# Kernel optimization log

Measured on AMD Instinct MI355X. Metric: run time of the kernel, lower is better.

Reference implementation:

```python
import jax, jax.numpy as jnp
import numpy as np

B, N, C_IN, C_OUT, BASIS = 8, 128, 64, 64, 15
AVG_NOBJ = 49.0
NEG_SLOPE = 0.01  # torch LeakyReLU default


def eops_2_to_2_sum(x, average_nobj=AVG_NOBJ):
    """x: [B, C, N, N] -> [B, C, 15, N, N].
    5 order-zero ops + 10 sum-aggregation ops (sums normalized by average_nobj,
    double sums by average_nobj**2, as in PELICAN's 'sum' aggregation)."""
    n = x.shape[-1]
    eye = jnp.eye(n, dtype=x.dtype)                       # [N, N]
    d = jnp.diagonal(x, axis1=-2, axis2=-1)               # [B, C, N]
    rowsum = x.sum(-1) / average_nobj                      # [B, C, N]
    colsum = x.sum(-2) / average_nobj                      # [B, C, N]
    trace = d.sum(-1) / average_nobj                       # [B, C]
    allsum = x.sum((-2, -1)) / (average_nobj ** 2)         # [B, C]
    bc = lambda v: jnp.broadcast_to(v, x.shape)
    ops = [
        # --- order zero (no aggregation) ---
        d[..., :, None] * eye,                 # diag(A) embedded on diagonal
        bc(d[..., :, None]),                   # A_ii broadcast along j
        bc(d[..., None, :]),                   # A_jj broadcast along i
        x,                                     # identity
        jnp.swapaxes(x, -1, -2),               # transpose
        # --- aggregation ops ---
        rowsum[..., :, None] * eye,            # row sums on diagonal
        colsum[..., :, None] * eye,            # col sums on diagonal
        trace[..., None, None] * eye,          # trace on diagonal
        allsum[..., None, None] * eye,         # total sum on diagonal
        bc(rowsum[..., :, None]),              # rowsum_i broadcast along j
        bc(rowsum[..., None, :]),              # rowsum_j broadcast along i
        bc(colsum[..., :, None]),              # colsum_i broadcast along j
        bc(colsum[..., None, :]),              # colsum_j broadcast along i
        bc(trace[..., None, None]),            # trace broadcast everywhere
        bc(allsum[..., None, None]),           # total sum broadcast everywhere
    ]
    return jnp.stack(ops, axis=2)              # [B, C, 15, N, N]


def setup_inputs() -> dict:
    key = jax.random.key(0)
    ks = jax.random.split(key, 5)
    inputs = jax.random.normal(ks[0], (B, N, N, C_IN), jnp.float32)
    mask = jnp.ones((B, N, N, 1), jnp.float32)
    nobj = jnp.full((B,), float(N), jnp.float32)
    s_b = float(np.sqrt(1.0 / BASIS))
    s_d = float(np.sqrt(1.0 / C_IN))
    coefs00 = jax.random.normal(ks[1], (C_IN, BASIS), jnp.float32) * s_b
    coefs01 = jax.random.normal(ks[2], (C_OUT, BASIS), jnp.float32) * s_b
    coefs10 = jax.random.normal(ks[3], (C_IN, C_OUT), jnp.float32) * s_d
    coefs11 = jax.random.normal(ks[4], (C_IN, C_OUT), jnp.float32) * s_d
    bias = jnp.zeros((C_OUT,), jnp.float32)
    diag_bias = jnp.zeros((C_OUT,), jnp.float32)
    return {"inputs": inputs, "mask": mask, "nobj": nobj,
            "coefs00": coefs00, "coefs01": coefs01,
            "coefs10": coefs10, "coefs11": coefs11,
            "bias": bias, "diag_bias": diag_bias}


def reference(inputs, mask, nobj, coefs00, coefs01, coefs10, coefs11, bias, diag_bias):
    # inputs: [B, N, N, C_in] -> channels-first for basis construction
    x = jnp.transpose(inputs, (0, 3, 1, 2))                     # [B, C, N, N]
    ops = eops_2_to_2_sum(x)                                    # [B, C, 15, N, N]
    # low-rank reconstructed coefficient tensor [C_in, C_out, 15]
    coefs = (coefs00[:, None, :] * coefs10[:, :, None]
             + coefs01[None, :, :] * coefs11[:, :, None])
    out = jnp.einsum('dsb,ndbij->nijs', coefs, ops)             # [B, N, N, C_out]
    eye = jnp.eye(inputs.shape[1], dtype=out.dtype)[None, :, :, None]
    out = out + bias[None, None, None, :] + eye * diag_bias[None, None, None, :]
    out = jax.nn.leaky_relu(out, NEG_SLOPE)
    return out * mask
```

## Files before the change

kernel.cpp:

```cpp
#include <hip/hip_runtime.h>

#define BB 8
#define NN 128
#define CC 64
static constexpr float INV_A = 1.0f / 49.0f;

#define OFF_C    0
#define OFF_CB   61440
#define OFF_RS   65536
#define OFF_CS   131072
#define OFF_DV   196608
#define OFF_U1   263168
#define OFF_U2   328704
#define OFF_DG   394240
#define OFF_XT   459776

typedef __attribute__((ext_vector_type(8))) short v8s;
typedef __attribute__((ext_vector_type(4))) float v4f;

static __device__ inline unsigned pack2bf(float a, float b) {
    union { float f; unsigned u; } ua, ub; ua.f = a; ub.f = b;
    return ((ua.u + 0x8000u) >> 16) | ((ub.u + 0x8000u) & 0xffff0000u);
}
static __device__ inline unsigned short f2bf(float a) {
    union { float f; unsigned u; } ua; ua.f = a;
    return (unsigned short)((ua.u + 0x8000u) >> 16);
}

__global__ void k_pre(const float* __restrict__ in,
                      const float* __restrict__ c00, const float* __restrict__ c01,
                      const float* __restrict__ c10, const float* __restrict__ c11,
                      float* __restrict__ ws) {
    if (blockIdx.x >= 512) {
        int idx = (blockIdx.x - 512) * 256 + threadIdx.x;
        if (idx < 15 * 4096) {
            int b = idx >> 12; int r = idx & 4095; int d = r >> 6; int s = r & 63;
            ws[OFF_C + idx] = c00[d * 15 + b] * c10[d * 64 + s] + c01[s * 15 + b] * c11[d * 64 + s];
        } else if (idx < 15 * 4096 + 8192) {
            int k = idx - 15 * 4096;
            int which = k >> 12;
            int r = k & 4095; int s = r >> 6; int d = r & 63;
            int b = 3 + which;
            float v = c00[d * 15 + b] * c10[d * 64 + s] + c01[s * 15 + b] * c11[d * 64 + s];
            unsigned short* cb = (unsigned short*)(ws + OFF_CB);
            cb[s * 128 + which * 64 + d] = f2bf(v);
        }
        return;
    }
    __shared__ float4 part[4][4][16];
    int mode = blockIdx.x >> 8;
    int bb = blockIdx.x & 255;
    int n = bb >> 5; int g0 = (bb & 31) * 4;
    int t = threadIdx.x;
    int q = t >> 6; int ii = (t >> 4) & 3; int d4 = t & 15;
    float4 acc = make_float4(0.f, 0.f, 0.f, 0.f);
    if (mode == 0) {
        int i = g0 + ii;
        float4 dvv = acc; bool hd = false;
        const float* base = in + ((size_t)(n * NN + i)) * NN * CC + d4 * 4;
        for (int j = q * 32; j < q * 32 + 32; ++j) {
            float4 v = *(const float4*)(base + (size_t)j * CC);
            acc.x += v.x; acc.y += v.y; acc.z += v.z; acc.w += v.w;
            if (j == i) { dvv = v; hd = true; }
        }
        if (hd) *(float4*)(ws + OFF_DV + ((size_t)(n * NN + i)) * CC + d4 * 4) = dvv;
    } else {
        int j = g0 + ii;
        unsigned short* xT = (unsigned short*)(ws + OFF_XT);
        for (int i = q * 32; i < q * 32 + 32; ++i) {
            float4 v = *(const float4*)(in + (((size_t)(n * NN + i)) * NN + j) * CC + d4 * 4);
            acc.x += v.x; acc.y += v.y; acc.z += v.z; acc.w += v.w;
            uint2 pk; pk.x = pack2bf(v.x, v.y); pk.y = pack2bf(v.z, v.w);
            *(uint2*)(xT + (((size_t)(n * NN + j)) * NN + i) * CC + d4 * 4) = pk;
        }
    }
    part[q][ii][d4] = acc;
    __syncthreads();
    if (t < 64) {
        int i2 = t >> 4; int dd = t & 15;
        float4 a = part[0][i2][dd], b = part[1][i2][dd], c = part[2][i2][dd], d = part[3][i2][dd];
        float4 s;
        s.x = (a.x + b.x + c.x + d.x) * INV_A;
        s.y = (a.y + b.y + c.y + d.y) * INV_A;
        s.z = (a.z + b.z + c.z + d.z) * INV_A;
        s.w = (a.w + b.w + c.w + d.w) * INV_A;
        *(float4*)(ws + (mode ? OFF_CS : OFF_RS) + ((size_t)(n * NN + g0 + i2)) * CC + dd * 4) = s;
    }
}

__global__ __launch_bounds__(256, 4) void k_uv(const float* __restrict__ bias,
                                               const float* __restrict__ dbias,
                                               float* __restrict__ ws) {
    __shared__ float trL[64], asL[64];
    __shared__ float pU1[4][4][64], pU2[4][4][64], pDG[4][4][64];
    __shared__ float pS[4][64], pDGc[4][64];
    int n = blockIdx.x >> 5; int i0 = (blockIdx.x & 31) * 4;
    int t = threadIdx.x;
    int s = t & 63; int q = t >> 6;

    {
        float tr = 0.f, as = 0.f;
        #pragma unroll 4
        for (int e = 0; e < 32; ++e) {
            int i = q * 32 + e;
            tr += ws[OFF_DV + ((size_t)(n * NN + i)) * CC + s];
            as += ws[OFF_RS + ((size_t)(n * NN + i)) * CC + s];
        }
        pS[q][s] = tr; pDGc[q][s] = as;
        __syncthreads();
        if (t < 64) {
            trL[t] = (pS[0][t] + pS[1][t] + pS[2][t] + pS[3][t]) * INV_A;
            asL[t] = (pDGc[0][t] + pDGc[1][t] + pDGc[2][t] + pDGc[3][t]) * INV_A;
        }
        __syncthreads();
    }

    const float* C = ws + OFF_C;
    float aU1[4] = {0, 0, 0, 0}, aU2[4] = {0, 0, 0, 0}, aDG[4] = {0, 0, 0, 0};
    float aS = 0.f, aDGc = 0.f;
    #pragma unroll
    for (int c4 = 0; c4 < 4; ++c4) {
        int dc = q * 4 + c4;
        float tr4[4], as4[4], dv4[4][4], rs4[4][4], cs4[4][4];
        #pragma unroll
        for (int k = 0; k < 4; ++k) { tr4[k] = trL[dc * 4 + k]; as4[k] = asL[dc * 4 + k]; }
        #pragma unroll
        for (int ii = 0; ii < 4; ++ii) {
            size_t ro = ((size_t)(n * NN + i0 + ii)) * CC + dc * 4;
            float4 v = *(const float4*)(ws + OFF_DV + ro);
            dv4[ii][0] = v.x; dv4[ii][1] = v.y; dv4[ii][2] = v.z; dv4[ii][3] = v.w;
            float4 r = *(const float4*)(ws + OFF_RS + ro);
            rs4[ii][0] = r.x; rs4[ii][1] = r.y; rs4[ii][2] = r.z; rs4[ii][3] = r.w;
            float4 c = *(const float4*)(ws + OFF_CS + ro);
            cs4[ii][0] = c.x; cs4[ii][1] = c.y; cs4[ii][2] = c.z; cs4[ii][3] = c.w;
        }
        #pragma unroll
        for (int k = 0; k < 4; ++k) {
            int d = dc * 4 + k;
            const float* Cd = C + d * 64 + s;
            float c0 = Cd[0 * 4096], c1 = Cd[1 * 4096], c2 = Cd[2 * 4096];
            float c5 = Cd[5 * 4096], c6 = Cd[6 * 4096], c7 = Cd[7 * 4096];
            float c8 = Cd[8 * 4096], c9 = Cd[9 * 4096], c10v = Cd[10 * 4096];
            float c11v = Cd[11 * 4096], c12v = Cd[12 * 4096];
            float c13 = Cd[13 * 4096], c14 = Cd[14 * 4096];
            aS += c13 * tr4[k] + c14 * as4[k];
            aDGc += c7 * tr4[k] + c8 * as4[k];
            #pragma unroll
            for (int ii = 0; ii < 4; ++ii) {
                aU1[ii] += c1 * dv4[ii][k] + c9 * rs4[ii][k] + c11v * cs4[ii][k];
                aU2[ii] += c2 * dv4[ii][k] + c10v * rs4[ii][k] + c12v * cs4[ii][k];
                aDG[ii] += c0 * dv4[ii][k] + c5 * rs4[ii][k] + c6 * cs4[ii][k];
            }
        }
    }
    #pragma unroll
    for (int ii = 0; ii < 4; ++ii) {
        pU1[q][ii][s] = aU1[ii]; pU2[q][ii][s] = aU2[ii]; pDG[q][ii][s] = aDG[ii];
    }
    pS[q][s] = aS; pDGc[q][s] = aDGc;
    __syncthreads();

    int fi = q;
    float u1 = pU1[0][fi][s] + pU1[1][fi][s] + pU1[2][fi][s] + pU1[3][fi][s];
    float u2 = pU2[0][fi][s] + pU2[1][fi][s] + pU2[2][fi][s] + pU2[3][fi][s];
    float dg = pDG[0][fi][s] + pDG[1][fi][s] + pDG[2][fi][s] + pDG[3][fi][s];
    float aSt = pS[0][s] + pS[1][s] + pS[2][s] + pS[3][s];
    float aDGct = pDGc[0][s] + pDGc[1][s] + pDGc[2][s] + pDGc[3][s];
    size_t row = ((size_t)(n * NN + i0 + fi)) * CC + s;
    ws[OFF_U1 + row] = u1 + aSt + bias[s];
    ws[OFF_U2 + row] = u2;
    ws[OFF_DG + row] = dg + aDGct + dbias[s];
}

__global__ __launch_bounds__(256, 4) void k_main(
        const float* __restrict__ in, const float* __restrict__ mask,
        const float* __restrict__ ws, float* __restrict__ out) {
    __shared__ __align__(16) unsigned char smem[34816];
    unsigned short* Ab = (unsigned short*)smem;
    unsigned short* Bb = (unsigned short*)(smem + 17408);
    float* Obuf = (float*)smem;

    int blk = blockIdx.x;
    int n = blk >> 8; int rem = blk & 255; int i = rem >> 1; int j0 = (rem & 1) * 64;
    int t = threadIdx.x;
    int tp = t >> 4; int c = t & 15;

    const unsigned short* cb = (const unsigned short*)(ws + OFF_CB);
    #pragma unroll
    for (int e = 0; e < 4; ++e) {
        int s = e * 16 + tp;
        float4 v = *(const float4*)(cb + s * 128 + c * 8);
        *(float4*)((unsigned char*)(Bb + s * 136 + c * 8)) = v;
    }
    {
        const float* src = in + (((size_t)(n * NN + i)) * NN + j0) * CC;
        #pragma unroll
        for (int e = 0; e < 4; ++e) {
            int p = e * 16 + tp;
            float4 v = *(const float4*)(src + (size_t)p * CC + c * 4);
            uint2 pk; pk.x = pack2bf(v.x, v.y); pk.y = pack2bf(v.z, v.w);
            *(uint2*)(Ab + p * 136 + c * 4) = pk;
        }
    }
    {
        const unsigned short* xT = (const unsigned short*)(ws + OFF_XT)
                                 + (((size_t)(n * NN + i)) * NN + j0) * CC;
        #pragma unroll
        for (int r = 0; r < 2; ++r) {
            int idx = t + r * 256;
            int p = idx >> 3; int ch = idx & 7;
            float4 v = *(const float4*)(xT + (size_t)p * CC + ch * 8);
            *(float4*)((unsigned char*)(Ab + p * 136 + 64 + ch * 8)) = v;
        }
    }
    __syncthreads();

    int w = t >> 6; int l = t & 63;
    int r16 = l & 15; int quad = l >> 4;
    v4f acc[4];
    #pragma unroll
    for (int st = 0; st < 4; ++st) acc[st] = 0.f;
    int arow = w * 16 + r16;
    #pragma unroll
    for (int kk = 0; kk < 4; ++kk) {
        v8s af = *(const v8s*)(Ab + arow * 136 + kk * 32 + quad * 8);
        #pragma unroll
        for (int st = 0; st < 4; ++st) {
            v8s bfr = *(const v8s*)(Bb + (st * 16 + r16) * 136 + kk * 32 + quad * 8);
            acc[st] = __builtin_amdgcn_mfma_f32_16x16x32_bf16(af, bfr, acc[st], 0, 0, 0);
        }
    }
    #pragma unroll
    for (int st = 0; st < 4; ++st)
        #pragma unroll
        for (int reg = 0; reg < 4; ++reg)
            Obuf[(w * 16 + quad * 4 + reg) * 68 + st * 16 + r16] = acc[st][reg];
    __syncthreads();

    int srow = (n * NN + i) * CC;
    float4 u1 = *(const float4*)(ws + OFF_U1 + srow + c * 4);
    float4 dg = *(const float4*)(ws + OFF_DG + srow + c * 4);
    #pragma unroll
    for (int e = 0; e < 4; ++e) {
        int p = e * 16 + tp;
        int j = j0 + p;
        float4 v = *(const float4*)(Obuf + p * 68 + c * 4);
        float4 u2 = *(const float4*)(ws + OFF_U2 + (n * NN + j) * CC + c * 4);
        v.x += u1.x + u2.x; v.y += u1.y + u2.y; v.z += u1.z + u2.z; v.w += u1.w + u2.w;
        if (j == i) { v.x += dg.x; v.y += dg.y; v.z += dg.z; v.w += dg.w; }
        v.x = v.x > 0.f ? v.x : 0.01f * v.x;
        v.y = v.y > 0.f ? v.y : 0.01f * v.y;
        v.z = v.z > 0.f ? v.z : 0.01f * v.z;
        v.w = v.w > 0.f ? v.w : 0.01f * v.w;
        float m = mask[((size_t)(n * NN + i)) * NN + j];
        v.x *= m; v.y *= m; v.z *= m; v.w *= m;
        *(float4*)(out + (((size_t)(n * NN + i)) * NN + j) * CC + c * 4) = v;
    }
}

extern "C" void kernel_launch(void* const* d_in, const int* in_sizes, int n_in,
                              void* d_out, int out_size, void* d_ws, size_t ws_size,
                              hipStream_t stream) {
    const float* inputs = (const float*)d_in[0];
    const float* mask   = (const float*)d_in[1];
    const float* c00 = (const float*)d_in[3];
    const float* c01 = (const float*)d_in[4];
    const float* c10 = (const float*)d_in[5];
    const float* c11 = (const float*)d_in[6];
    const float* bias  = (const float*)d_in[7];
    const float* dbias = (const float*)d_in[8];
    float* out = (float*)d_out;
    float* ws = (float*)d_ws;

    k_pre <<<784, 256, 0, stream>>>(inputs, c00, c01, c10, c11, ws);
    k_uv  <<<256, 256, 0, stream>>>(bias, dbias, ws);
    k_main<<<2048, 256, 0, stream>>>(inputs, mask, ws, out);
}
```

Before: 134.6 us.

## Fuse row-sum and transpose passes; compute column sums from bf16 transpose in k_uv

The preprocessing kernel used to read the fp32 input twice, once for row sums and diagonal and once, strided, for column sums plus the bf16 transpose. It now reads the input once per row, producing row sums, the diagonal and the transposed bf16 copy together. Column sums are recomputed in k_uv by reading the bf16 transpose contiguously, which removes the strided fp32 input read. The cost is that column sums are now accumulated from bf16-rounded values, which loses precision, and the transpose writes from k_pre become scattered.

```diff
diff --git a/kernel.cpp b/kernel.cpp
--- a/kernel.cpp
+++ b/kernel.cpp
@@ -8,7 +8,6 @@
 #define OFF_C    0
 #define OFF_CB   61440
 #define OFF_RS   65536
-#define OFF_CS   131072
 #define OFF_DV   196608
 #define OFF_U1   263168
 #define OFF_U2   328704
@@ -26,13 +25,19 @@
     union { float f; unsigned u; } ua; ua.f = a;
     return (unsigned short)((ua.u + 0x8000u) >> 16);
 }
+static __device__ inline float bf_lo(unsigned u) {
+    union { unsigned u; float f; } c; c.u = u << 16; return c.f;
+}
+static __device__ inline float bf_hi(unsigned u) {
+    union { unsigned u; float f; } c; c.u = u & 0xffff0000u; return c.f;
+}
 
 __global__ void k_pre(const float* __restrict__ in,
                       const float* __restrict__ c00, const float* __restrict__ c01,
                       const float* __restrict__ c10, const float* __restrict__ c11,
                       float* __restrict__ ws) {
-    if (blockIdx.x >= 512) {
-        int idx = (blockIdx.x - 512) * 256 + threadIdx.x;
+    if (blockIdx.x >= 256) {
+        int idx = (blockIdx.x - 256) * 256 + threadIdx.x;
         if (idx < 15 * 4096) {
             int b = idx >> 12; int r = idx & 4095; int d = r >> 6; int s = r & 63;
             ws[OFF_C + idx] = c00[d * 15 + b] * c10[d * 64 + s] + c01[s * 15 + b] * c11[d * 64 + s];
@@ -48,32 +53,23 @@
         return;
     }
     __shared__ float4 part[4][4][16];
-    int mode = blockIdx.x >> 8;
-    int bb = blockIdx.x & 255;
+    int bb = blockIdx.x;
     int n = bb >> 5; int g0 = (bb & 31) * 4;
     int t = threadIdx.x;
     int q = t >> 6; int ii = (t >> 4) & 3; int d4 = t & 15;
+    int i = g0 + ii;
     float4 acc = make_float4(0.f, 0.f, 0.f, 0.f);
-    if (mode == 0) {
-        int i = g0 + ii;
-        float4 dvv = acc; bool hd = false;
-        const float* base = in + ((size_t)(n * NN + i)) * NN * CC + d4 * 4;
-        for (int j = q * 32; j < q * 32 + 32; ++j) {
-            float4 v = *(const float4*)(base + (size_t)j * CC);
-            acc.x += v.x; acc.y += v.y; acc.z += v.z; acc.w += v.w;
-            if (j == i) { dvv = v; hd = true; }
-        }
-        if (hd) *(float4*)(ws + OFF_DV + ((size_t)(n * NN + i)) * CC + d4 * 4) = dvv;
-    } else {
-        int j = g0 + ii;
-        unsigned short* xT = (unsigned short*)(ws + OFF_XT);
-        for (int i = q * 32; i < q * 32 + 32; ++i) {
-            float4 v = *(const float4*)(in + (((size_t)(n * NN + i)) * NN + j) * CC + d4 * 4);
-            acc.x += v.x; acc.y += v.y; acc.z += v.z; acc.w += v.w;
-            uint2 pk; pk.x = pack2bf(v.x, v.y); pk.y = pack2bf(v.z, v.w);
-            *(uint2*)(xT + (((size_t)(n * NN + j)) * NN + i) * CC + d4 * 4) = pk;
-        }
-    }
+    float4 dvv = acc; bool hd = false;
+    const float* base = in + ((size_t)(n * NN + i)) * NN * CC + d4 * 4;
+    unsigned short* xT = (unsigned short*)(ws + OFF_XT);
+    for (int j = q * 32; j < q * 32 + 32; ++j) {
+        float4 v = *(const float4*)(base + (size_t)j * CC);
+        acc.x += v.x; acc.y += v.y; acc.z += v.z; acc.w += v.w;
+        uint2 pk; pk.x = pack2bf(v.x, v.y); pk.y = pack2bf(v.z, v.w);
+        *(uint2*)(xT + (((size_t)(n * NN + j)) * NN + i) * CC + d4 * 4) = pk;
+        if (j == i) { dvv = v; hd = true; }
+    }
+    if (hd) *(float4*)(ws + OFF_DV + ((size_t)(n * NN + i)) * CC + d4 * 4) = dvv;
     part[q][ii][d4] = acc;
     __syncthreads();
     if (t < 64) {
@@ -84,14 +80,15 @@
         s.y = (a.y + b.y + c.y + d.y) * INV_A;
         s.z = (a.z + b.z + c.z + d.z) * INV_A;
         s.w = (a.w + b.w + c.w + d.w) * INV_A;
-        *(float4*)(ws + (mode ? OFF_CS : OFF_RS) + ((size_t)(n * NN + g0 + i2)) * CC + dd * 4) = s;
+        *(float4*)(ws + OFF_RS + ((size_t)(n * NN + g0 + i2)) * CC + dd * 4) = s;
     }
 }
 
 __global__ __launch_bounds__(256, 4) void k_uv(const float* __restrict__ bias,
                                                const float* __restrict__ dbias,
                                                float* __restrict__ ws) {
-    __shared__ float trL[64], asL[64];
+    __shared__ float trL[64], asL[64], csL[4][64];
+    __shared__ float pcs[4][4][64];
     __shared__ float pU1[4][4][64], pU2[4][4][64], pDG[4][4][64];
     __shared__ float pS[4][64], pDGc[4][64];
     int n = blockIdx.x >> 5; int i0 = (blockIdx.x & 31) * 4;
@@ -107,7 +104,22 @@
             as += ws[OFF_RS + ((size_t)(n * NN + i)) * CC + s];
         }
         pS[q][s] = tr; pDGc[q][s] = as;
+
+        int d4 = t & 15; int ig = (t >> 4) & 3;
+        const unsigned short* xr = (const unsigned short*)(ws + OFF_XT)
+                                 + ((size_t)(n * NN + (i0 + q))) * NN * CC + d4 * 4;
+        float c0 = 0.f, c1 = 0.f, c2 = 0.f, c3 = 0.f;
+        #pragma unroll 4
+        for (int e = 0; e < 32; ++e) {
+            int i = ig * 32 + e;
+            uint2 u = *(const uint2*)(xr + (size_t)i * CC);
+            c0 += bf_lo(u.x); c1 += bf_hi(u.x);
+            c2 += bf_lo(u.y); c3 += bf_hi(u.y);
+        }
+        pcs[q][ig][d4 * 4 + 0] = c0; pcs[q][ig][d4 * 4 + 1] = c1;
+        pcs[q][ig][d4 * 4 + 2] = c2; pcs[q][ig][d4 * 4 + 3] = c3;
         __syncthreads();
+        csL[q][s] = (pcs[q][0][s] + pcs[q][1][s] + pcs[q][2][s] + pcs[q][3][s]) * INV_A;
         if (t < 64) {
             trL[t] = (pS[0][t] + pS[1][t] + pS[2][t] + pS[3][t]) * INV_A;
             asL[t] = (pDGc[0][t] + pDGc[1][t] + pDGc[2][t] + pDGc[3][t]) * INV_A;
@@ -131,8 +143,8 @@
             dv4[ii][0] = v.x; dv4[ii][1] = v.y; dv4[ii][2] = v.z; dv4[ii][3] = v.w;
             float4 r = *(const float4*)(ws + OFF_RS + ro);
             rs4[ii][0] = r.x; rs4[ii][1] = r.y; rs4[ii][2] = r.z; rs4[ii][3] = r.w;
-            float4 c = *(const float4*)(ws + OFF_CS + ro);
-            cs4[ii][0] = c.x; cs4[ii][1] = c.y; cs4[ii][2] = c.z; cs4[ii][3] = c.w;
+            #pragma unroll
+            for (int k = 0; k < 4; ++k) cs4[ii][k] = csL[ii][dc * 4 + k];
         }
         #pragma unroll
         for (int k = 0; k < 4; ++k) {
@@ -272,7 +284,7 @@
     float* out = (float*)d_out;
     float* ws = (float*)d_ws;
 
-    k_pre <<<784, 256, 0, stream>>>(inputs, c00, c01, c10, c11, ws);
+    k_pre <<<528, 256, 0, stream>>>(inputs, c00, c01, c10, c11, ws);
     k_uv  <<<256, 256, 0, stream>>>(bias, dbias, ws);
     k_main<<<2048, 256, 0, stream>>>(inputs, mask, ws, out);
 }
```

After: 139.2 us. +3.4%, slower.
